# Kernel tuning notes

Measured on AMD Instinct MI355X. Metric: run time of the kernel, lower is better.

Reference implementation:

```python
import jax, jax.numpy as jnp
import numpy as np

B, N, C, H = 16, 4096, 384, 8
NH = N // H  # per-head patch chunk = 512


def setup_inputs() -> dict:
    key = jax.random.key(0)
    ks = jax.random.split(key, 5)
    s = 1.0 / np.sqrt(N)
    return {
        "x": jax.random.normal(ks[0], (B, N, C), dtype=jnp.float32),
        "wq": jax.random.normal(ks[1], (N, N), dtype=jnp.float32) * s,
        "wkv": jax.random.normal(ks[2], (2 * N, N), dtype=jnp.float32) * s,
        "wproj": jax.random.normal(ks[3], (N, N), dtype=jnp.float32) * s,
        "bproj": jax.random.normal(ks[4], (N,), dtype=jnp.float32) * s,
        "scale": jnp.ones((H, 1, 1), dtype=jnp.float32),
    }


def reference(x, wq, wkv, wproj, bproj, scale):
    # x: [B, N, C] -> token-mixing over patch dim N
    xt = jnp.swapaxes(x, -2, -1)                      # [B, C, N]
    q = jnp.einsum('bcn,mn->bcm', xt, wq)             # [B, C, N]
    kv = jnp.einsum('bcn,mn->bcm', xt, wkv)           # [B, C, 2N]
    q = q.reshape(B, C, H, NH).transpose(0, 2, 1, 3)  # [B, H, C, NH]
    kv = kv.reshape(B, C, 2, H, NH).transpose(2, 0, 3, 1, 4)  # [2, B, H, C, NH]
    k, v = kv[0], kv[1]
    q = q / jnp.linalg.norm(q, axis=-1, keepdims=True)
    k = k / jnp.linalg.norm(k, axis=-1, keepdims=True)
    # channel-reduction kernel trick: [B, H, 1, NH], scaled per head
    kernel_trick = (k * v).sum(axis=-2, keepdims=True) * scale
    o = q * kernel_trick                               # [B, H, C, NH]
    o = o.transpose(0, 2, 1, 3).reshape(B, C, N)       # [B, C, N]
    o = jax.nn.gelu(o, approximate=False)              # torch nn.GELU = exact erf
    o = jnp.einsum('bcn,mn->bcm', o, wproj) + bproj    # proj over patch dim
    return jnp.swapaxes(o, -2, -1)                     # [B, N, C]
```

## Files before the change

kernel.cpp:

```cpp
#include <hip/hip_runtime.h>
#include <hip/hip_bf16.h>
#include <math.h>
#include <stdint.h>

#define B_ 16
#define N_ 4096
#define C_ 384
#define H_ 8
#define NH_ 512

typedef __attribute__((ext_vector_type(8))) short short8;
typedef __attribute__((ext_vector_type(4))) float f32x4;

__device__ __forceinline__ unsigned short f2bf(float x) {
  uint32_t u = __builtin_bit_cast(uint32_t, x);
  uint32_t r = (u + 0x7fffu + ((u >> 16) & 1u)) >> 16;
  return (unsigned short)r;
}
__device__ __forceinline__ float bf2f(unsigned short u) {
  uint32_t v = ((uint32_t)u) << 16;
  return __builtin_bit_cast(float, v);
}

__device__ __forceinline__ void gl2lds16(const void* g, void* l) {
  __builtin_amdgcn_global_load_lds((__attribute__((address_space(1))) void*)g,
                                   (__attribute__((address_space(3))) void*)l,
                                   16, 0, 0);
}

__global__ void cvt_f32_bf16(const float* __restrict__ src,
                             unsigned short* __restrict__ dst, size_t n) {
  size_t i = ((size_t)blockIdx.x * blockDim.x + threadIdx.x) * 8;
  if (i >= n) return;
  float4 a = *(const float4*)(src + i);
  float4 b = *(const float4*)(src + i + 4);
  typedef __attribute__((ext_vector_type(8))) unsigned short u16x8;
  u16x8 o;
  o[0] = f2bf(a.x); o[1] = f2bf(a.y); o[2] = f2bf(a.z); o[3] = f2bf(a.w);
  o[4] = f2bf(b.x); o[5] = f2bf(b.y); o[6] = f2bf(b.z); o[7] = f2bf(b.w);
  *(u16x8*)(dst + i) = o;
}

__global__ __launch_bounds__(256)
void transpose_x(const float* __restrict__ x, unsigned short* __restrict__ xT) {
  __shared__ float tile[64 * 65];
  int b = blockIdx.z;
  int n0 = blockIdx.x * 64;
  int c0 = blockIdx.y * 64;
  int t = threadIdx.x;
  const float* xb = x + (size_t)b * N_ * C_;
  #pragma unroll
  for (int i = 0; i < 16; i++) {
    int r = i * 4 + (t >> 6);
    int cc = t & 63;
    tile[r * 65 + cc] = xb[(size_t)(n0 + r) * C_ + c0 + cc];
  }
  __syncthreads();
  unsigned short* xTb = xT + (size_t)b * C_ * N_;
  #pragma unroll
  for (int i = 0; i < 16; i++) {
    int r = i * 4 + (t >> 6);
    int nn = t & 63;
    xTb[(size_t)(c0 + r) * N_ + n0 + nn] = f2bf(tile[nn * 65 + r]);
  }
}

template <bool BIAS>
__global__ __launch_bounds__(512, 4)
void gemm_bt(const unsigned short* __restrict__ A,
             const unsigned short* __restrict__ Bt,
             void* __restrict__ OutV,
             const float* __restrict__ bias,
             size_t outBatchStride) {
  __shared__ unsigned short As[256 * 64];
  __shared__ unsigned short Bs[128 * 64];
  const int ct = blockIdx.x;
  const int m0 = blockIdx.y * 256;
  const int cg0 = ct * 128;
  const int t = threadIdx.x;
  const int lane = t & 63;
  const int w = t >> 6;
  const int wm = (w & 3) * 64;
  const int wn = (w >> 2) * 64;
  const int quad = lane >> 4;
  const int r16  = lane & 15;

  f32x4 acc[4][4];
  #pragma unroll
  for (int i = 0; i < 4; i++)
    #pragma unroll
    for (int j = 0; j < 4; j++)
      acc[i][j] = (f32x4){0.f, 0.f, 0.f, 0.f};

  const int rs = t >> 3;
  const int q8 = (t & 7) ^ (rs & 7);
  const unsigned short* aSrc = A  + (size_t)(m0 + rs) * 4096 + q8 * 8;
  const unsigned short* bSrc = Bt + (size_t)(cg0 + rs) * 4096 + q8 * 8;
  unsigned short* aDst = As + t * 8;
  unsigned short* bDst = Bs + t * 8;

  for (int k0 = 0; k0 < 4096; k0 += 64) {
    #pragma unroll
    for (int p = 0; p < 4; p++)
      gl2lds16(aSrc + (size_t)p * 64 * 4096 + k0, aDst + p * 4096);
    #pragma unroll
    for (int p = 0; p < 2; p++)
      gl2lds16(bSrc + (size_t)p * 64 * 4096 + k0, bDst + p * 4096);
    __syncthreads();
    #pragma unroll
    for (int kk = 0; kk < 2; kk++) {
      short8 af[4], bfv[4];
      const int cb = kk * 4 + quad;
      #pragma unroll
      for (int i = 0; i < 4; i++) {
        int ra = wm + i * 16 + r16;
        af[i]  = *(const short8*)(As + ra * 64 + ((cb ^ (ra & 7)) * 8));
        int rb = wn + i * 16 + r16;
        bfv[i] = *(const short8*)(Bs + rb * 64 + ((cb ^ (rb & 7)) * 8));
      }
      #pragma unroll
      for (int i = 0; i < 4; i++)
        #pragma unroll
        for (int j = 0; j < 4; j++)
          acc[i][j] = __builtin_amdgcn_mfma_f32_16x16x32_bf16(
              af[i], bfv[j], acc[i][j], 0, 0, 0);
    }
    __syncthreads();
  }

  const int bb = ct / 3;
  const int cbase = (ct - bb * 3) * 128;

  if (BIAS) {
    float* Out = (float*)OutV + (size_t)bb * outBatchStride;
    #pragma unroll
    for (int i = 0; i < 4; i++) {
      #pragma unroll
      for (int v = 0; v < 4; v++) {
        int m = m0 + wm + i * 16 + quad * 4 + v;
        float bi = bias[m];
        #pragma unroll
        for (int j = 0; j < 4; j++) {
          int c = cbase + wn + j * 16 + r16;
          Out[(size_t)m * C_ + c] = acc[i][j][v] + bi;
        }
      }
    }
  } else {
    unsigned short* Out = (unsigned short*)OutV + (size_t)bb * outBatchStride;
    #pragma unroll
    for (int i = 0; i < 4; i++) {
      #pragma unroll
      for (int v = 0; v < 4; v++) {
        int m = m0 + wm + i * 16 + quad * 4 + v;
        #pragma unroll
        for (int j = 0; j < 4; j++) {
          int c = cbase + wn + j * 16 + r16;
          Out[(size_t)m * C_ + c] = f2bf(acc[i][j][v]);
        }
      }
    }
  }
}

__global__ __launch_bounds__(512)
void middle(const unsigned short* __restrict__ Y,
            unsigned short* __restrict__ GT,
            const float* __restrict__ scale) {
  const int h = blockIdx.x;
  const int b = blockIdx.y;
  const unsigned short* Yb = Y + (size_t)b * 12288 * C_;
  const unsigned short* Q = Yb + (size_t)(h * NH_) * C_;
  const unsigned short* K = Yb + (size_t)(N_ + h * NH_) * C_;
  const unsigned short* V = Yb + (size_t)(2 * N_ + h * NH_) * C_;
  unsigned short* GTb = GT + (size_t)b * C_ * N_ + h * NH_;

  __shared__ float invq[C_], invk[C_], kt[NH_];
  const int t = threadIdx.x;
  const float sc = scale[h];

  if (t < C_) {
    float sq = 0.f, sk = 0.f;
    for (int n = 0; n < NH_; n++) {
      float qv = bf2f(Q[(size_t)n * C_ + t]);
      float kv = bf2f(K[(size_t)n * C_ + t]);
      sq += qv * qv;
      sk += kv * kv;
    }
    invq[t] = rsqrtf(sq);
    invk[t] = rsqrtf(sk);
  }
  __syncthreads();

  {
    int w = t >> 6, l = t & 63;
    for (int n = w; n < NH_; n += 8) {
      float s = 0.f;
      for (int c = l; c < C_; c += 64)
        s += bf2f(K[(size_t)n * C_ + c]) * invk[c] * bf2f(V[(size_t)n * C_ + c]);
      #pragma unroll
      for (int o = 32; o > 0; o >>= 1) s += __shfl_xor(s, o);
      if (l == 0) kt[n] = s * sc;
    }
  }
  __syncthreads();

  {
    int n = t;
    float ktv = kt[n];
    for (int c = 0; c < C_; c++) {
      float xv = bf2f(Q[(size_t)n * C_ + c]) * invq[c] * ktv;
      float g = 0.5f * xv * (1.0f + erff(xv * 0.70710678118654752f));
      GTb[(size_t)c * N_ + n] = f2bf(g);
    }
  }
}

extern "C" void kernel_launch(void* const* d_in, const int* in_sizes, int n_in,
                              void* d_out, int out_size, void* d_ws, size_t ws_size,
                              hipStream_t stream) {
  const float* x     = (const float*)d_in[0];
  const float* wq    = (const float*)d_in[1];
  const float* wkv   = (const float*)d_in[2];
  const float* wproj = (const float*)d_in[3];
  const float* bproj = (const float*)d_in[4];
  const float* scale = (const float*)d_in[5];

  unsigned short* Wqkv = (unsigned short*)d_ws;
  unsigned short* Wp   = Wqkv + (size_t)12288 * 4096;
  unsigned short* xT   = Wp   + (size_t)4096 * 4096;
  unsigned short* Y    = xT   + (size_t)B_ * C_ * N_;
  unsigned short* GT   = Y    + (size_t)B_ * 12288 * C_;

  const size_t nq  = (size_t)4096 * 4096;
  const size_t nkv = (size_t)8192 * 4096;

  cvt_f32_bf16<<<(int)(nq  / 8 / 256), 256, 0, stream>>>(wq,    Wqkv,      nq);
  cvt_f32_bf16<<<(int)(nkv / 8 / 256), 256, 0, stream>>>(wkv,   Wqkv + nq, nkv);
  cvt_f32_bf16<<<(int)(nq  / 8 / 256), 256, 0, stream>>>(wproj, Wp,        nq);

  transpose_x<<<dim3(64, 6, 16), 256, 0, stream>>>(x, xT);

  gemm_bt<false><<<dim3(48, 48), 512, 0, stream>>>(
      Wqkv, xT, Y, nullptr, (size_t)12288 * C_);

  middle<<<dim3(8, 16), 512, 0, stream>>>(Y, GT, scale);

  gemm_bt<true><<<dim3(48, 16), 512, 0, stream>>>(
      Wp, GT, d_out, bproj, (size_t)N_ * C_);
}
```

Measured before the change: 1.442 ms.

## Use 32x32 MFMA with smaller GEMM tiles and split middle into coalesced kernels

The GEMM kernel moves from 256x128 tiles with 8 waves of 16x16x32 MFMAs to 128x128 tiles with 4 waves of 32x32x16 MFMAs. This doubles the number of blocks and cuts per-wave fragment loads from LDS. The middle kernel is split in two. One kernel computes the norms and the kernel-trick vector, and a new tiled kernel applies GELU across many more blocks, transposing through LDS so the GT writes are coalesced. The old version had poor parallelism with only 128 blocks and strided stores. In exchange the change adds a launch, global scratch for invq and kt, and less operand reuse per block.

```diff
diff --git a/kernel.cpp b/kernel.cpp
--- a/kernel.cpp
+++ b/kernel.cpp
@@ -11,6 +11,7 @@
 
 typedef __attribute__((ext_vector_type(8))) short short8;
 typedef __attribute__((ext_vector_type(4))) float f32x4;
+typedef __attribute__((ext_vector_type(16))) float f32x16;
 
 __device__ __forceinline__ unsigned short f2bf(float x) {
   uint32_t u = __builtin_bit_cast(uint32_t, x);
@@ -66,31 +67,31 @@
 }
 
 template <bool BIAS>
-__global__ __launch_bounds__(512, 4)
+__global__ __launch_bounds__(256, 4)
 void gemm_bt(const unsigned short* __restrict__ A,
              const unsigned short* __restrict__ Bt,
              void* __restrict__ OutV,
              const float* __restrict__ bias,
              size_t outBatchStride) {
-  __shared__ unsigned short As[256 * 64];
+  __shared__ unsigned short As[128 * 64];
   __shared__ unsigned short Bs[128 * 64];
   const int ct = blockIdx.x;
-  const int m0 = blockIdx.y * 256;
+  const int m0 = blockIdx.y * 128;
   const int cg0 = ct * 128;
   const int t = threadIdx.x;
   const int lane = t & 63;
   const int w = t >> 6;
-  const int wm = (w & 3) * 64;
-  const int wn = (w >> 2) * 64;
-  const int quad = lane >> 4;
-  const int r16  = lane & 15;
-
-  f32x4 acc[4][4];
-  #pragma unroll
-  for (int i = 0; i < 4; i++)
-    #pragma unroll
-    for (int j = 0; j < 4; j++)
-      acc[i][j] = (f32x4){0.f, 0.f, 0.f, 0.f};
+  const int wm = (w & 1) * 64;
+  const int wn = (w >> 1) * 64;
+  const int l31 = lane & 31;
+  const int lh  = lane >> 5;
+
+  f32x16 acc[2][2];
+  #pragma unroll
+  for (int i = 0; i < 2; i++)
+    #pragma unroll
+    for (int j = 0; j < 2; j++)
+      acc[i][j] = (f32x16){0.f};
 
   const int rs = t >> 3;
   const int q8 = (t & 7) ^ (rs & 7);
@@ -101,28 +102,27 @@
 
   for (int k0 = 0; k0 < 4096; k0 += 64) {
     #pragma unroll
-    for (int p = 0; p < 4; p++)
-      gl2lds16(aSrc + (size_t)p * 64 * 4096 + k0, aDst + p * 4096);
-    #pragma unroll
-    for (int p = 0; p < 2; p++)
-      gl2lds16(bSrc + (size_t)p * 64 * 4096 + k0, bDst + p * 4096);
+    for (int p = 0; p < 4; p++) {
+      gl2lds16(aSrc + (size_t)p * 32 * 4096 + k0, aDst + p * 2048);
+      gl2lds16(bSrc + (size_t)p * 32 * 4096 + k0, bDst + p * 2048);
+    }
     __syncthreads();
     #pragma unroll
-    for (int kk = 0; kk < 2; kk++) {
-      short8 af[4], bfv[4];
-      const int cb = kk * 4 + quad;
-      #pragma unroll
-      for (int i = 0; i < 4; i++) {
-        int ra = wm + i * 16 + r16;
+    for (int ks = 0; ks < 4; ks++) {
+      short8 af[2], bfv[2];
+      const int cb = ks * 2 + lh;
+      #pragma unroll
+      for (int i = 0; i < 2; i++) {
+        int ra = wm + i * 32 + l31;
         af[i]  = *(const short8*)(As + ra * 64 + ((cb ^ (ra & 7)) * 8));
-        int rb = wn + i * 16 + r16;
+        int rb = wn + i * 32 + l31;
         bfv[i] = *(const short8*)(Bs + rb * 64 + ((cb ^ (rb & 7)) * 8));
       }
       #pragma unroll
-      for (int i = 0; i < 4; i++)
+      for (int i = 0; i < 2; i++)
         #pragma unroll
-        for (int j = 0; j < 4; j++)
-          acc[i][j] = __builtin_amdgcn_mfma_f32_16x16x32_bf16(
+        for (int j = 0; j < 2; j++)
+          acc[i][j] = __builtin_amdgcn_mfma_f32_32x32x16_bf16(
               af[i], bfv[j], acc[i][j], 0, 0, 0);
     }
     __syncthreads();
@@ -134,29 +134,31 @@
   if (BIAS) {
     float* Out = (float*)OutV + (size_t)bb * outBatchStride;
     #pragma unroll
-    for (int i = 0; i < 4; i++) {
-      #pragma unroll
-      for (int v = 0; v < 4; v++) {
-        int m = m0 + wm + i * 16 + quad * 4 + v;
+    for (int i = 0; i < 2; i++) {
+      #pragma unroll
+      for (int r = 0; r < 16; r++) {
+        int rr = (r & 3) + 8 * (r >> 2) + 4 * lh;
+        int m = m0 + wm + i * 32 + rr;
         float bi = bias[m];
         #pragma unroll
-        for (int j = 0; j < 4; j++) {
-          int c = cbase + wn + j * 16 + r16;
-          Out[(size_t)m * C_ + c] = acc[i][j][v] + bi;
+        for (int j = 0; j < 2; j++) {
+          int c = cbase + wn + j * 32 + l31;
+          Out[(size_t)m * C_ + c] = acc[i][j][r] + bi;
         }
       }
     }
   } else {
     unsigned short* Out = (unsigned short*)OutV + (size_t)bb * outBatchStride;
     #pragma unroll
-    for (int i = 0; i < 4; i++) {
-      #pragma unroll
-      for (int v = 0; v < 4; v++) {
-        int m = m0 + wm + i * 16 + quad * 4 + v;
+    for (int i = 0; i < 2; i++) {
+      #pragma unroll
+      for (int r = 0; r < 16; r++) {
+        int rr = (r & 3) + 8 * (r >> 2) + 4 * lh;
+        int m = m0 + wm + i * 32 + rr;
         #pragma unroll
-        for (int j = 0; j < 4; j++) {
-          int c = cbase + wn + j * 16 + r16;
-          Out[(size_t)m * C_ + c] = f2bf(acc[i][j][v]);
+        for (int j = 0; j < 2; j++) {
+          int c = cbase + wn + j * 32 + l31;
+          Out[(size_t)m * C_ + c] = f2bf(acc[i][j][r]);
         }
       }
     }
@@ -164,30 +166,29 @@
 }
 
 __global__ __launch_bounds__(512)
-void middle(const unsigned short* __restrict__ Y,
-            unsigned short* __restrict__ GT,
-            const float* __restrict__ scale) {
+void middle_norms(const unsigned short* __restrict__ Y,
+                  float* __restrict__ invq, float* __restrict__ kt,
+                  const float* __restrict__ scale) {
   const int h = blockIdx.x;
   const int b = blockIdx.y;
   const unsigned short* Yb = Y + (size_t)b * 12288 * C_;
   const unsigned short* Q = Yb + (size_t)(h * NH_) * C_;
   const unsigned short* K = Yb + (size_t)(N_ + h * NH_) * C_;
   const unsigned short* V = Yb + (size_t)(2 * N_ + h * NH_) * C_;
-  unsigned short* GTb = GT + (size_t)b * C_ * N_ + h * NH_;
-
-  __shared__ float invq[C_], invk[C_], kt[NH_];
   const int t = threadIdx.x;
   const float sc = scale[h];
+  __shared__ float invk[C_];
 
   if (t < C_) {
     float sq = 0.f, sk = 0.f;
+    #pragma unroll 8
     for (int n = 0; n < NH_; n++) {
       float qv = bf2f(Q[(size_t)n * C_ + t]);
       float kv = bf2f(K[(size_t)n * C_ + t]);
       sq += qv * qv;
       sk += kv * kv;
     }
-    invq[t] = rsqrtf(sq);
+    invq[((size_t)(b * 8 + h)) * C_ + t] = rsqrtf(sq);
     invk[t] = rsqrtf(sk);
   }
   __syncthreads();
@@ -200,19 +201,49 @@
         s += bf2f(K[(size_t)n * C_ + c]) * invk[c] * bf2f(V[(size_t)n * C_ + c]);
       #pragma unroll
       for (int o = 32; o > 0; o >>= 1) s += __shfl_xor(s, o);
-      if (l == 0) kt[n] = s * sc;
-    }
-  }
-  __syncthreads();
-
-  {
-    int n = t;
-    float ktv = kt[n];
-    for (int c = 0; c < C_; c++) {
-      float xv = bf2f(Q[(size_t)n * C_ + c]) * invq[c] * ktv;
-      float g = 0.5f * xv * (1.0f + erff(xv * 0.70710678118654752f));
-      GTb[(size_t)c * N_ + n] = f2bf(g);
-    }
+      if (l == 0) kt[((size_t)(b * 8 + h)) * NH_ + n] = s * sc;
+    }
+  }
+}
+
+__global__ __launch_bounds__(256)
+void middle_apply(const unsigned short* __restrict__ Y,
+                  const float* __restrict__ invq, const float* __restrict__ kt,
+                  unsigned short* __restrict__ GT) {
+  const int nt = blockIdx.x & 7;
+  const int ctile = blockIdx.x >> 3;
+  const int h = blockIdx.y;
+  const int b = blockIdx.z;
+  const int n0 = nt * 64;
+  const int c0 = ctile * 64;
+  const unsigned short* Q = Y + (size_t)b * 12288 * C_ + (size_t)(h * NH_) * C_;
+  const int t = threadIdx.x;
+
+  __shared__ unsigned short tile[64 * 65];
+  __shared__ float invqs[64], kts[64];
+  if (t < 64) invqs[t] = invq[((size_t)(b * 8 + h)) * C_ + c0 + t];
+  else if (t < 128) kts[t - 64] = kt[((size_t)(b * 8 + h)) * NH_ + n0 + (t - 64)];
+  __syncthreads();
+
+  #pragma unroll
+  for (int i = 0; i < 16; i++) {
+    int idx = i * 256 + t;
+    int r = idx >> 6;
+    int cc = idx & 63;
+    float q = bf2f(Q[(size_t)(n0 + r) * C_ + c0 + cc]);
+    float xv = q * invqs[cc] * kts[r];
+    float g = 0.5f * xv * (1.0f + erff(xv * 0.70710678118654752f));
+    tile[cc * 65 + r] = f2bf(g);
+  }
+  __syncthreads();
+
+  unsigned short* GTb = GT + ((size_t)b * C_ + c0) * N_ + h * NH_ + n0;
+  #pragma unroll
+  for (int i = 0; i < 16; i++) {
+    int idx = i * 256 + t;
+    int cc = idx >> 6;
+    int r = idx & 63;
+    GTb[(size_t)cc * N_ + r] = tile[cc * 65 + r];
   }
 }
 
@@ -231,6 +262,8 @@
   unsigned short* xT   = Wp   + (size_t)4096 * 4096;
   unsigned short* Y    = xT   + (size_t)B_ * C_ * N_;
   unsigned short* GT   = Y    + (size_t)B_ * 12288 * C_;
+  float* invq = (float*)(GT + (size_t)B_ * C_ * N_);
+  float* kt   = invq + (size_t)B_ * H_ * C_;
 
   const size_t nq  = (size_t)4096 * 4096;
   const size_t nkv = (size_t)8192 * 4096;
@@ -241,11 +274,12 @@
 
   transpose_x<<<dim3(64, 6, 16), 256, 0, stream>>>(x, xT);
 
-  gemm_bt<false><<<dim3(48, 48), 512, 0, stream>>>(
+  gemm_bt<false><<<dim3(48, 96), 256, 0, stream>>>(
       Wqkv, xT, Y, nullptr, (size_t)12288 * C_);
 
-  middle<<<dim3(8, 16), 512, 0, stream>>>(Y, GT, scale);
-
-  gemm_bt<true><<<dim3(48, 16), 512, 0, stream>>>(
+  middle_norms<<<dim3(8, 16), 512, 0, stream>>>(Y, invq, kt, scale);
+  middle_apply<<<dim3(48, 8, 16), 256, 0, stream>>>(Y, invq, kt, GT);
+
+  gemm_bt<true><<<dim3(48, 32), 256, 0, stream>>>(
       Wp, GT, d_out, bproj, (size_t)N_ * C_);
 }
```

Result: no change. 1.456 ms (+0.9%).
